# Kernel optimization log

Measured on AMD Instinct MI355X. Metric: run time of the kernel, lower is better.

Reference implementation:

```python
import jax, jax.numpy as jnp
import numpy as np

B, S, D, H, FFN = 4, 1024, 1024, 16, 4096
DH = D // H
EPS = 1e-5
NEG = -1e20


def _layer_norm(t, g, b):
    m = jnp.mean(t, axis=-1, keepdims=True)
    v = jnp.mean((t - m) ** 2, axis=-1, keepdims=True)
    return (t - m) / jnp.sqrt(v + EPS) * g + b


def setup_inputs() -> dict:
    key = jax.random.key(0)
    ks = jax.random.split(key, 16)
    std_attn = np.sqrt(2.0 / (D + D)).astype(np.float32)  # xavier normal
    lim1 = np.sqrt(6.0 / (D + FFN)).astype(np.float32)    # xavier uniform
    inp = {
        'tensor': jax.random.normal(ks[0], (B, S, D), jnp.float32),
        'mask': jnp.ones((B, S), jnp.int32),
        'wq': jax.random.normal(ks[1], (D, D), jnp.float32) * std_attn,
        'bq': jnp.zeros((D,), jnp.float32),
        'wk': jax.random.normal(ks[2], (D, D), jnp.float32) * std_attn,
        'bk': jnp.zeros((D,), jnp.float32),
        'wv': jax.random.normal(ks[3], (D, D), jnp.float32) * std_attn,
        'bv': jnp.zeros((D,), jnp.float32),
        'wo': jax.random.normal(ks[4], (D, D), jnp.float32) * std_attn,
        'bo': jnp.zeros((D,), jnp.float32),
        'ln1_g': jnp.ones((D,), jnp.float32),
        'ln1_b': jnp.zeros((D,), jnp.float32),
        'w1': jax.random.uniform(ks[5], (FFN, D), jnp.float32, -lim1, lim1),
        'b1': jnp.zeros((FFN,), jnp.float32),
        'w2': jax.random.uniform(ks[6], (D, FFN), jnp.float32, -lim1, lim1),
        'b2': jnp.zeros((D,), jnp.float32),
        'ln2_g': jnp.ones((D,), jnp.float32),
        'ln2_b': jnp.zeros((D,), jnp.float32),
    }
    return inp


def reference(tensor, mask, wq, bq, wk, bk, wv, bv, wo, bo,
              ln1_g, ln1_b, w1, b1, w2, b2, ln2_g, ln2_b):
    x = tensor
    scale = jnp.sqrt(jnp.float32(DH))
    # QKV projections -> [B, S, H, DH]
    q = (x @ wq.T + bq).reshape(B, S, H, DH)
    k = (x @ wk.T + bk).reshape(B, S, H, DH)
    v = (x @ wv.T + bv).reshape(B, S, H, DH)
    # scores [B, H, Sq, Sk]
    scores = jnp.einsum('bqhd,bkhd->bhqk', q / scale, k)
    blocked = (mask == 0)[:, None, None, :]  # True -> block
    scores = jnp.where(blocked, NEG, scores)
    attn = jax.nn.softmax(scores.astype(jnp.float32), axis=-1).astype(x.dtype)
    ctx = jnp.einsum('bhqk,bkhd->bqhd', attn, v).reshape(B, S, D)
    attn_out = ctx @ wo.T + bo
    # post-LN (variant='aiayn')
    t = _layer_norm(x + attn_out, ln1_g, ln1_b)
    ffn = jax.nn.relu(t @ w1.T + b1) @ w2.T + b2
    t = _layer_norm(t + ffn, ln2_g, ln2_b)
    t = t * mask[:, :, None].astype(t.dtype)
    return t
```

## Files before the change

### kernel.cpp

```cpp
#include <hip/hip_runtime.h>

typedef __bf16 bf16x8 __attribute__((ext_vector_type(8)));
typedef __bf16 bf16x4 __attribute__((ext_vector_type(4)));
typedef float f32x4 __attribute__((ext_vector_type(4)));
typedef float f32x16 __attribute__((ext_vector_type(16)));

#define BB 4
#define SS 1024
#define DD 1024
#define HH 16
#define DHH 64
#define FFN 4096

__device__ __forceinline__ void gload_lds16(const void* g, void* lds) {
  __builtin_amdgcn_global_load_lds(
      (const __attribute__((address_space(1))) unsigned int*)g,
      (__attribute__((address_space(3))) unsigned int*)lds, 16, 0, 0);
}

__global__ __launch_bounds__(256) void cvt_all_kernel(
    const float* __restrict__ x, const float* __restrict__ wq, const float* __restrict__ wk,
    const float* __restrict__ wv, const float* __restrict__ wo, const float* __restrict__ w1,
    const float* __restrict__ w2, __bf16* __restrict__ xb, __bf16* __restrict__ wqkvb,
    __bf16* __restrict__ wob, __bf16* __restrict__ w1b, __bf16* __restrict__ w2b)
{
  int i = blockIdx.x * 256 + threadIdx.x;
  const float* src; __bf16* dst; int off;
  if (i < 524288)       { src = x;  dst = xb;              off = i; }
  else if (i < 655360)  { src = wq; dst = wqkvb;           off = i - 524288; }
  else if (i < 786432)  { src = wk; dst = wqkvb + 1048576; off = i - 655360; }
  else if (i < 917504)  { src = wv; dst = wqkvb + 2097152; off = i - 786432; }
  else if (i < 1048576) { src = wo; dst = wob;             off = i - 917504; }
  else if (i < 1572864) { src = w1; dst = w1b;             off = i - 1048576; }
  else                  { src = w2; dst = w2b;             off = i - 1572864; }
  float4 a = *(const float4*)(src + off * 8);
  float4 b = *(const float4*)(src + off * 8 + 4);
  bf16x8 v;
  v[0] = (__bf16)a.x; v[1] = (__bf16)a.y; v[2] = (__bf16)a.z; v[3] = (__bf16)a.w;
  v[4] = (__bf16)b.x; v[5] = (__bf16)b.y; v[6] = (__bf16)b.z; v[7] = (__bf16)b.w;
  *(bf16x8*)(dst + off * 8) = v;
}

template<int MODE>
__global__ __launch_bounds__(256, 2) void gemm_bt(
    const __bf16* __restrict__ A, const __bf16* __restrict__ Bw,
    const float* __restrict__ bias, const float* __restrict__ bias1, const float* __restrict__ bias2,
    const float* __restrict__ res, void* __restrict__ outp, void* __restrict__ out1,
    int M, int N, int K, int kLen, float scale)
{
  __shared__ __bf16 As[2][128 * 32];
  __shared__ __bf16 Bs[2][128 * 32];
  const int tid = threadIdx.x;
  const int wid = tid >> 6;
  const int lane = tid & 63;
  const int lr = lane & 15;
  const int lg = lane >> 4;

  const int gx = gridDim.x;
  const int nwg = gx * gridDim.y;
  const int wg = blockIdx.y * gx + blockIdx.x;
  const int swz = (wg & 7) * (nwg >> 3) + (wg >> 3);
  const int bm = (swz / gx) * 128;
  const int bn = (swz % gx) * 128;

  const int wm = (wid >> 1) * 64;
  const int wn = (wid & 1) * 64;

  int kBeg = 0, nk = K >> 5;
  if constexpr (MODE == 5) { kBeg = blockIdx.z * kLen; nk = kLen >> 5; }

  const int off = tid * 16;
  const int srow = off >> 6;
  const int scol = (off & 63) >> 1;
  const __bf16* gA0 = A + (size_t)(bm + srow) * K + kBeg + scol;
  const __bf16* gA1 = A + (size_t)(bm + 64 + srow) * K + kBeg + scol;
  const __bf16* gB0 = Bw + (size_t)(bn + srow) * K + kBeg + scol;
  const __bf16* gB1 = Bw + (size_t)(bn + 64 + srow) * K + kBeg + scol;
  char* lA = (char*)&As[0][0] + wid * 1024;
  char* lB = (char*)&Bs[0][0] + wid * 1024;

  f32x4 acc[4][4] = {};

#define STAGE(buf, kk) do { \
    gload_lds16(gA0 + (kk), lA + (buf) * 8192); \
    gload_lds16(gA1 + (kk), lA + (buf) * 8192 + 4096); \
    gload_lds16(gB0 + (kk), lB + (buf) * 8192); \
    gload_lds16(gB1 + (kk), lB + (buf) * 8192 + 4096); \
  } while (0)

  STAGE(0, 0);
  __syncthreads();
  for (int t = 0; t < nk; ++t) {
    const int cur = t & 1;
    if (t + 1 < nk) STAGE(cur ^ 1, (t + 1) << 5);
    bf16x8 af[4], bv[4];
#pragma unroll
    for (int i = 0; i < 4; ++i)
      af[i] = *(const bf16x8*)&As[cur][(wm + i * 16 + lr) * 32 + lg * 8];
#pragma unroll
    for (int i = 0; i < 4; ++i)
      bv[i] = *(const bf16x8*)&Bs[cur][(wn + i * 16 + lr) * 32 + lg * 8];
#pragma unroll
    for (int i = 0; i < 4; ++i)
#pragma unroll
      for (int j = 0; j < 4; ++j)
        acc[i][j] = __builtin_amdgcn_mfma_f32_16x16x32_bf16(af[i], bv[j], acc[i][j], 0, 0, 0);
    __syncthreads();
  }
#undef STAGE

#pragma unroll
  for (int i = 0; i < 4; ++i) {
#pragma unroll
    for (int j = 0; j < 4; ++j) {
#pragma unroll
      for (int r = 0; r < 4; ++r) {
        int row = bm + wm + i * 16 + lg * 4 + r;
        int col = bn + wn + j * 16 + lr;
        float v = acc[i][j][r];
        if constexpr (MODE == 3) {
          float t2 = v + bias[col];
          ((__bf16*)outp)[(size_t)row * N + col] = (__bf16)fmaxf(t2, 0.f);
        } else if constexpr (MODE == 4) {
          int region = col >> 10;
          int col_ = col & 1023;
          int b_ = row >> 10, s_ = row & 1023;
          int h_ = col_ >> 6, d_ = col_ & 63;
          if (region == 0) {
            float v2 = (v + bias[col_]) * scale;
            ((__bf16*)outp)[(((size_t)(b_ * HH + h_) * SS) + s_) * DHH + d_] = (__bf16)v2;
          } else if (region == 1) {
            float v2 = v + bias1[col_];
            ((__bf16*)out1)[(((size_t)(b_ * HH + h_) * SS) + s_) * DHH + d_] = (__bf16)v2;
          } else {
            float v2 = v + bias2[col_];
            ((__bf16*)res)[(((size_t)(b_ * HH + h_) * DHH) + d_) * SS + s_] = (__bf16)v2;
          }
        } else if constexpr (MODE == 5) {
          float* dst = blockIdx.z ? (float*)out1 : (float*)outp;
          dst[(size_t)row * N + col] = v;
        } else if constexpr (MODE == 6) {
          size_t idx = (size_t)row * N + col;
          ((__bf16*)outp)[idx] = (__bf16)(v + bias[col] + res[idx]);
        }
      }
    }
  }
}

__global__ __launch_bounds__(256, 2) void attn_kernel(
    const __bf16* __restrict__ q, const __bf16* __restrict__ k,
    const __bf16* __restrict__ vt, const int* __restrict__ mask,
    __bf16* __restrict__ ctx)
{
  const int nwg = gridDim.x;
  const int wg = blockIdx.x;
  const int swzb = (wg & 7) * (nwg >> 3) + (wg >> 3);
  const int bh = swzb >> 3;
  const int qb = (swzb & 7) << 7;
  const int b = bh >> 4;

  const int tid = threadIdx.x, wid = tid >> 6, lane = tid & 63;
  const int ln = lane & 31, hi = lane >> 5;

  __shared__ __bf16 Kt[2][64 * 64];
  __shared__ __bf16 Vt[2][64 * 64];
  __shared__ __bf16 Pt[4][32 * 64];
  __shared__ float mmulLds[SS];

  {
    const int* mrow = mask + b * SS;
    int c = tid * 4;
    float4 mm;
    mm.x = (float)(mrow[c + 0] != 0);
    mm.y = (float)(mrow[c + 1] != 0);
    mm.z = (float)(mrow[c + 2] != 0);
    mm.w = (float)(mrow[c + 3] != 0);
    ((float4*)mmulLds)[tid] = mm;
  }

  const __bf16* qh = q + (size_t)bh * SS * DHH;
  const __bf16* kh = k + (size_t)bh * SS * DHH;
  const __bf16* vh = vt + (size_t)bh * DHH * SS;

  const int qw = qb + wid * 32;
  bf16x8 qf[4];
#pragma unroll
  for (int s = 0; s < 4; ++s)
    qf[s] = *(const bf16x8*)&qh[(size_t)(qw + ln) * DHH + s * 16 + hi * 8];

  const int srow = tid >> 3;
  const int ps = tid & 7;
  const int sw0 = (srow ^ (srow >> 3)) & 7;
  const int r1 = srow + 32;
  const int sw1 = (r1 ^ (r1 >> 3)) & 7;
  const __bf16* kS0 = kh + (size_t)srow * DHH + ((ps ^ sw0) * 8);
  const __bf16* kS1 = kh + (size_t)r1 * DHH + ((ps ^ sw1) * 8);
  const __bf16* vS0 = vh + (size_t)srow * SS + ((ps ^ sw0) * 8);
  const __bf16* vS1 = vh + (size_t)r1 * SS + ((ps ^ sw1) * 8);

#define ASTAGE(bufi, kb_) do { \
    gload_lds16(kS0 + (size_t)(kb_) * DHH, (char*)&Kt[bufi][0] + wid * 1024); \
    gload_lds16(kS1 + (size_t)(kb_) * DHH, (char*)&Kt[bufi][0] + wid * 1024 + 4096); \
    gload_lds16(vS0 + (kb_), (char*)&Vt[bufi][0] + wid * 1024); \
    gload_lds16(vS1 + (kb_), (char*)&Vt[bufi][0] + wid * 1024 + 4096); \
  } while (0)

  char* Pw = (char*)&Pt[wid][0];
  const int swA = (ln ^ (ln >> 3)) & 7;
  const int swB = swA ^ 4;

  f32x16 o0 = {}, o1 = {};
  float l[16];
#pragma unroll
  for (int r = 0; r < 16; ++r) l[r] = 0.f;

  ASTAGE(0, 0);
  __syncthreads();

#pragma unroll 1
  for (int t = 0; t < SS / 64; ++t) {
    const int cur = t & 1;
    const int kb = t * 64;
    if (t + 1 < SS / 64) ASTAGE(cur ^ 1, kb + 64);

    const char* Kc = (const char*)&Kt[cur][0];
    const char* Vc = (const char*)&Vt[cur][0];

    f32x16 sc0 = {}, sc1 = {};
#pragma unroll
    for (int s = 0; s < 4; ++s) {
      bf16x8 kb0 = *(const bf16x8*)(Kc + ln * 128 + (((s * 2 + hi) ^ swA) << 4));
      bf16x8 kb1 = *(const bf16x8*)(Kc + (32 + ln) * 128 + (((s * 2 + hi) ^ swB) << 4));
      sc0 = __builtin_amdgcn_mfma_f32_32x32x16_bf16(qf[s], kb0, sc0, 0, 0, 0);
      sc1 = __builtin_amdgcn_mfma_f32_32x32x16_bf16(qf[s], kb1, sc1, 0, 0, 0);
    }

    float mm0 = mmulLds[kb + ln];
    float mm1 = mmulLds[kb + 32 + ln];
#pragma unroll
    for (int r = 0; r < 16; ++r) {
      float p0 = exp2f(sc0[r] - 23.0831207f) * mm0;
      float p1 = exp2f(sc1[r] - 23.0831207f) * mm1;
      l[r] += p0 + p1;
      int qrow = (r & 3) + 8 * (r >> 2) + 4 * hi;
      int swq = (qrow ^ (qrow >> 3)) & 7;
      *(__bf16*)(Pw + qrow * 128 + ((((ln >> 3) + 0) ^ swq) << 4) + (ln & 7) * 2) = (__bf16)p0;
      *(__bf16*)(Pw + qrow * 128 + ((((ln >> 3) + 4) ^ swq) << 4) + (ln & 7) * 2) = (__bf16)p1;
    }

#pragma unroll
    for (int ks = 0; ks < 4; ++ks) {
      bf16x8 pa = *(const bf16x8*)(Pw + ln * 128 + (((ks * 2 + hi) ^ swA) << 4));
      bf16x8 vb0 = *(const bf16x8*)(Vc + ln * 128 + (((ks * 2 + hi) ^ swA) << 4));
      bf16x8 vb1 = *(const bf16x8*)(Vc + (32 + ln) * 128 + (((ks * 2 + hi) ^ swB) << 4));
      o0 = __builtin_amdgcn_mfma_f32_32x32x16_bf16(pa, vb0, o0, 0, 0, 0);
      o1 = __builtin_amdgcn_mfma_f32_32x32x16_bf16(pa, vb1, o1, 0, 0, 0);
    }
    __syncthreads();
  }
#undef ASTAGE

#pragma unroll
  for (int r = 0; r < 16; ++r) {
#pragma unroll
    for (int off = 1; off < 32; off <<= 1) l[r] += __shfl_xor(l[r], off);
  }

#pragma unroll
  for (int r = 0; r < 16; ++r) {
    float inv = l[r] > 0.f ? 1.f / l[r] : 0.f;
    int qrow = (r & 3) + 8 * (r >> 2) + 4 * hi;
    size_t base = ((size_t)b * SS + qw + qrow) * DD + (size_t)(bh & 15) * DHH;
    ctx[base + ln] = (__bf16)(o0[r] * inv);
    ctx[base + 32 + ln] = (__bf16)(o1[r] * inv);
  }
}

__global__ __launch_bounds__(256) void ln_bf16_kernel(
    const __bf16* __restrict__ in, const float* __restrict__ g, const float* __restrict__ b,
    __bf16* __restrict__ out16)
{
  int row = blockIdx.x;
  int tid = threadIdx.x;
  int wid = tid >> 6, lane = tid & 63;
  bf16x4 raw = ((const bf16x4*)(in + (size_t)row * DD))[tid];
  float4 v;
  v.x = (float)raw[0]; v.y = (float)raw[1]; v.z = (float)raw[2]; v.w = (float)raw[3];
  float s = v.x + v.y + v.z + v.w;
  float sq = v.x * v.x + v.y * v.y + v.z * v.z + v.w * v.w;
#pragma unroll
  for (int o = 1; o < 64; o <<= 1) { s += __shfl_xor(s, o); sq += __shfl_xor(sq, o); }
  __shared__ float red[8];
  if (lane == 0) { red[wid] = s; red[4 + wid] = sq; }
  __syncthreads();
  s = red[0] + red[1] + red[2] + red[3];
  sq = red[4] + red[5] + red[6] + red[7];
  float mean = s * (1.f / DD);
  float var = sq * (1.f / DD) - mean * mean;
  float rstd = rsqrtf(var + 1e-5f);
  float4 gg = ((const float4*)g)[tid];
  float4 bb = ((const float4*)b)[tid];
  bf16x4 w;
  w[0] = (__bf16)((v.x - mean) * rstd * gg.x + bb.x);
  w[1] = (__bf16)((v.y - mean) * rstd * gg.y + bb.y);
  w[2] = (__bf16)((v.z - mean) * rstd * gg.z + bb.z);
  w[3] = (__bf16)((v.w - mean) * rstd * gg.w + bb.w);
  *(bf16x4*)(out16 + (size_t)row * DD + tid * 4) = w;
}

__global__ __launch_bounds__(256) void ln2_fused_kernel(
    const float* __restrict__ p0, const float* __restrict__ p1, const float* __restrict__ bias,
    const __bf16* __restrict__ res, const float* __restrict__ g, const float* __restrict__ b,
    const int* __restrict__ mask, float* __restrict__ out)
{
  int row = blockIdx.x;
  int tid = threadIdx.x;
  int wid = tid >> 6, lane = tid & 63;
  size_t base = (size_t)row * DD;
  float4 a0 = ((const float4*)(p0 + base))[tid];
  float4 a1 = ((const float4*)(p1 + base))[tid];
  bf16x4 rw = ((const bf16x4*)(res + base))[tid];
  float4 bs = ((const float4*)bias)[tid];
  float4 v;
  v.x = a0.x + a1.x + (float)rw[0] + bs.x;
  v.y = a0.y + a1.y + (float)rw[1] + bs.y;
  v.z = a0.z + a1.z + (float)rw[2] + bs.z;
  v.w = a0.w + a1.w + (float)rw[3] + bs.w;
  float s = v.x + v.y + v.z + v.w;
  float sq = v.x * v.x + v.y * v.y + v.z * v.z + v.w * v.w;
#pragma unroll
  for (int o = 1; o < 64; o <<= 1) { s += __shfl_xor(s, o); sq += __shfl_xor(sq, o); }
  __shared__ float red[8];
  if (lane == 0) { red[wid] = s; red[4 + wid] = sq; }
  __syncthreads();
  s = red[0] + red[1] + red[2] + red[3];
  sq = red[4] + red[5] + red[6] + red[7];
  float mean = s * (1.f / DD);
  float var = sq * (1.f / DD) - mean * mean;
  float rstd = rsqrtf(var + 1e-5f);
  float4 gg = ((const float4*)g)[tid];
  float4 bb = ((const float4*)b)[tid];
  float mk = (float)mask[row];
  float4 o;
  o.x = ((v.x - mean) * rstd * gg.x + bb.x) * mk;
  o.y = ((v.y - mean) * rstd * gg.y + bb.y) * mk;
  o.z = ((v.z - mean) * rstd * gg.z + bb.z) * mk;
  o.w = ((v.w - mean) * rstd * gg.w + bb.w) * mk;
  ((float4*)(out + base))[tid] = o;
}

extern "C" void kernel_launch(void* const* d_in, const int* in_sizes, int n_in,
                              void* d_out, int out_size, void* d_ws, size_t ws_size,
                              hipStream_t stream) {
  const float* x    = (const float*)d_in[0];
  const int*  mask  = (const int*)d_in[1];
  const float* wq   = (const float*)d_in[2];
  const float* bq   = (const float*)d_in[3];
  const float* wk   = (const float*)d_in[4];
  const float* bk   = (const float*)d_in[5];
  const float* wv   = (const float*)d_in[6];
  const float* bv   = (const float*)d_in[7];
  const float* wo   = (const float*)d_in[8];
  const float* bo   = (const float*)d_in[9];
  const float* ln1g = (const float*)d_in[10];
  const float* ln1b = (const float*)d_in[11];
  const float* w1   = (const float*)d_in[12];
  const float* b1   = (const float*)d_in[13];
  const float* w2   = (const float*)d_in[14];
  const float* b2   = (const float*)d_in[15];
  const float* ln2g = (const float*)d_in[16];
  const float* ln2b = (const float*)d_in[17];
  float* out = (float*)d_out;
  char* ws = (char*)d_ws;

  __bf16* xb    = (__bf16*)(ws + 0);
  __bf16* wqkvb = (__bf16*)(ws + 8388608);
  __bf16* wob   = (__bf16*)(ws + 14680064);
  __bf16* w1b   = (__bf16*)(ws + 16777216);
  __bf16* w2b   = (__bf16*)(ws + 25165824);
  __bf16* qbuf  = (__bf16*)(ws + 33554432);
  __bf16* kbuf  = (__bf16*)(ws + 41943040);
  __bf16* vtbf  = (__bf16*)(ws + 50331648);
  __bf16* ctxb  = (__bf16*)(ws + 58720256);
  __bf16* hb    = (__bf16*)(ws + 33554432);
  __bf16* r1b   = (__bf16*)(ws + 67108864);
  float*  p0    = (float*)(ws + 83886080);
  __bf16* tb    = (__bf16*)(ws + 100663296);
  float*  p1    = (float*)(ws + 0);

  const int MSD = BB * SS;

  cvt_all_kernel<<<8192, 256, 0, stream>>>(x, wq, wk, wv, wo, w1, w2, xb, wqkvb, wob, w1b, w2b);

  gemm_bt<4><<<dim3(24, 32), 256, 0, stream>>>(xb, wqkvb, bq, bk, bv, (const float*)vtbf,
                                               qbuf, kbuf, MSD, 3072, DD, 0, 0.18033688f);

  attn_kernel<<<BB * HH * (SS / 128), 256, 0, stream>>>(qbuf, kbuf, vtbf, mask, ctxb);

  gemm_bt<6><<<dim3(8, 32), 256, 0, stream>>>(ctxb, wob, bo, nullptr, nullptr, x,
                                              r1b, nullptr, MSD, DD, DD, 0, 1.0f);
  ln_bf16_kernel<<<MSD, 256, 0, stream>>>(r1b, ln1g, ln1b, tb);

  gemm_bt<3><<<dim3(32, 32), 256, 0, stream>>>(tb, w1b, b1, nullptr, nullptr, nullptr,
                                               hb, nullptr, MSD, FFN, DD, 0, 1.0f);

  gemm_bt<5><<<dim3(8, 32, 2), 256, 0, stream>>>(hb, w2b, nullptr, nullptr, nullptr, nullptr,
                                                 p0, p1, MSD, DD, FFN, 2048, 1.0f);
  ln2_fused_kernel<<<MSD, 256, 0, stream>>>(p0, p1, b2, tb, ln2g, ln2b, mask, out);
}
```

Measured before the change: 231.9 us.

## Widen GEMM tiles to 128x256 with 512-thread blocks for QKV and FFN

Adds a gemm_wide kernel using 8 waves per block and a 128x256 output tile, with the B tile doubled in LDS. It is used for the QKV, FFN1 and FFN2 GEMMs to raise A-tile reuse and cut global traffic per FLOP. The output-projection GEMM keeps the old 128x128 tile as a separate gemm_wo kernel. The trade-off is fewer workgroups (for example 256 for FFN2), more LDS per block and possibly lower occupancy or uneven load across CUs.

Result: slower. 242.5 us (+4.6%).

```diff
diff --git a/kernel.cpp b/kernel.cpp
--- a/kernel.cpp
+++ b/kernel.cpp
@@ -42,14 +42,14 @@
 }
 
 template<int MODE>
-__global__ __launch_bounds__(256, 2) void gemm_bt(
+__global__ __launch_bounds__(512, 2) void gemm_wide(
     const __bf16* __restrict__ A, const __bf16* __restrict__ Bw,
     const float* __restrict__ bias, const float* __restrict__ bias1, const float* __restrict__ bias2,
     const float* __restrict__ res, void* __restrict__ outp, void* __restrict__ out1,
     int M, int N, int K, int kLen, float scale)
 {
   __shared__ __bf16 As[2][128 * 32];
-  __shared__ __bf16 Bs[2][128 * 32];
+  __shared__ __bf16 Bs[2][256 * 32];
   const int tid = threadIdx.x;
   const int wid = tid >> 6;
   const int lane = tid & 63;
@@ -61,31 +61,28 @@
   const int wg = blockIdx.y * gx + blockIdx.x;
   const int swz = (wg & 7) * (nwg >> 3) + (wg >> 3);
   const int bm = (swz / gx) * 128;
-  const int bn = (swz % gx) * 128;
-
-  const int wm = (wid >> 1) * 64;
-  const int wn = (wid & 1) * 64;
+  const int bn = (swz % gx) * 256;
+
+  const int wm = (wid >> 2) * 64;
+  const int wn = (wid & 3) * 64;
 
   int kBeg = 0, nk = K >> 5;
   if constexpr (MODE == 5) { kBeg = blockIdx.z * kLen; nk = kLen >> 5; }
 
-  const int off = tid * 16;
-  const int srow = off >> 6;
-  const int scol = (off & 63) >> 1;
-  const __bf16* gA0 = A + (size_t)(bm + srow) * K + kBeg + scol;
-  const __bf16* gA1 = A + (size_t)(bm + 64 + srow) * K + kBeg + scol;
-  const __bf16* gB0 = Bw + (size_t)(bn + srow) * K + kBeg + scol;
-  const __bf16* gB1 = Bw + (size_t)(bn + 64 + srow) * K + kBeg + scol;
+  const int sra = tid >> 2;
+  const int sca = (tid & 3) << 3;
+  const __bf16* gA  = A + (size_t)(bm + sra) * K + kBeg + sca;
+  const __bf16* gB0 = Bw + (size_t)(bn + sra) * K + kBeg + sca;
+  const __bf16* gB1 = Bw + (size_t)(bn + 128 + sra) * K + kBeg + sca;
   char* lA = (char*)&As[0][0] + wid * 1024;
   char* lB = (char*)&Bs[0][0] + wid * 1024;
 
   f32x4 acc[4][4] = {};
 
 #define STAGE(buf, kk) do { \
-    gload_lds16(gA0 + (kk), lA + (buf) * 8192); \
-    gload_lds16(gA1 + (kk), lA + (buf) * 8192 + 4096); \
-    gload_lds16(gB0 + (kk), lB + (buf) * 8192); \
-    gload_lds16(gB1 + (kk), lB + (buf) * 8192 + 4096); \
+    gload_lds16(gA + (kk), lA + (buf) * 8192); \
+    gload_lds16(gB0 + (kk), lB + (buf) * 16384); \
+    gload_lds16(gB1 + (kk), lB + (buf) * 16384 + 8192); \
   } while (0)
 
   STAGE(0, 0);
@@ -139,7 +136,88 @@
         } else if constexpr (MODE == 5) {
           float* dst = blockIdx.z ? (float*)out1 : (float*)outp;
           dst[(size_t)row * N + col] = v;
-        } else if constexpr (MODE == 6) {
+        }
+      }
+    }
+  }
+}
+
+template<int MODE>
+__global__ __launch_bounds__(256, 2) void gemm_wo(
+    const __bf16* __restrict__ A, const __bf16* __restrict__ Bw,
+    const float* __restrict__ bias, const float* __restrict__ res,
+    void* __restrict__ outp, int M, int N, int K)
+{
+  __shared__ __bf16 As[2][128 * 32];
+  __shared__ __bf16 Bs[2][128 * 32];
+  const int tid = threadIdx.x;
+  const int wid = tid >> 6;
+  const int lane = tid & 63;
+  const int lr = lane & 15;
+  const int lg = lane >> 4;
+
+  const int gx = gridDim.x;
+  const int nwg = gx * gridDim.y;
+  const int wg = blockIdx.y * gx + blockIdx.x;
+  const int swz = (wg & 7) * (nwg >> 3) + (wg >> 3);
+  const int bm = (swz / gx) * 128;
+  const int bn = (swz % gx) * 128;
+
+  const int wm = (wid >> 1) * 64;
+  const int wn = (wid & 1) * 64;
+
+  const int nk = K >> 5;
+
+  const int off = tid * 16;
+  const int srow = off >> 6;
+  const int scol = (off & 63) >> 1;
+  const __bf16* gA0 = A + (size_t)(bm + srow) * K + scol;
+  const __bf16* gA1 = A + (size_t)(bm + 64 + srow) * K + scol;
+  const __bf16* gB0 = Bw + (size_t)(bn + srow) * K + scol;
+  const __bf16* gB1 = Bw + (size_t)(bn + 64 + srow) * K + scol;
+  char* lA = (char*)&As[0][0] + wid * 1024;
+  char* lB = (char*)&Bs[0][0] + wid * 1024;
+
+  f32x4 acc[4][4] = {};
+
+#define STAGE(buf, kk) do { \
+    gload_lds16(gA0 + (kk), lA + (buf) * 8192); \
+    gload_lds16(gA1 + (kk), lA + (buf) * 8192 + 4096); \
+    gload_lds16(gB0 + (kk), lB + (buf) * 8192); \
+    gload_lds16(gB1 + (kk), lB + (buf) * 8192 + 4096); \
+  } while (0)
+
+  STAGE(0, 0);
+  __syncthreads();
+  for (int t = 0; t < nk; ++t) {
+    const int cur = t & 1;
+    if (t + 1 < nk) STAGE(cur ^ 1, (t + 1) << 5);
+    bf16x8 af[4], bv[4];
+#pragma unroll
+    for (int i = 0; i < 4; ++i)
+      af[i] = *(const bf16x8*)&As[cur][(wm + i * 16 + lr) * 32 + lg * 8];
+#pragma unroll
+    for (int i = 0; i < 4; ++i)
+      bv[i] = *(const bf16x8*)&Bs[cur][(wn + i * 16 + lr) * 32 + lg * 8];
+#pragma unroll
+    for (int i = 0; i < 4; ++i)
+#pragma unroll
+      for (int j = 0; j < 4; ++j)
+        acc[i][j] = __builtin_amdgcn_mfma_f32_16x16x32_bf16(af[i], bv[j], acc[i][j], 0, 0, 0);
+    __syncthreads();
+  }
+#undef STAGE
+
+#pragma unroll
+  for (int i = 0; i < 4; ++i) {
+#pragma unroll
+    for (int j = 0; j < 4; ++j) {
+#pragma unroll
+      for (int r = 0; r < 4; ++r) {
+        int row = bm + wm + i * 16 + lg * 4 + r;
+        int col = bn + wn + j * 16 + lr;
+        float v = acc[i][j][r];
+        if constexpr (MODE == 6) {
           size_t idx = (size_t)row * N + col;
           ((__bf16*)outp)[idx] = (__bf16)(v + bias[col] + res[idx]);
         }
@@ -393,19 +471,18 @@
 
   cvt_all_kernel<<<8192, 256, 0, stream>>>(x, wq, wk, wv, wo, w1, w2, xb, wqkvb, wob, w1b, w2b);
 
-  gemm_bt<4><<<dim3(24, 32), 256, 0, stream>>>(xb, wqkvb, bq, bk, bv, (const float*)vtbf,
-                                               qbuf, kbuf, MSD, 3072, DD, 0, 0.18033688f);
+  gemm_wide<4><<<dim3(12, 32), 512, 0, stream>>>(xb, wqkvb, bq, bk, bv, (const float*)vtbf,
+                                                 qbuf, kbuf, MSD, 3072, DD, 0, 0.18033688f);
 
   attn_kernel<<<BB * HH * (SS / 128), 256, 0, stream>>>(qbuf, kbuf, vtbf, mask, ctxb);
 
-  gemm_bt<6><<<dim3(8, 32), 256, 0, stream>>>(ctxb, wob, bo, nullptr, nullptr, x,
-                                              r1b, nullptr, MSD, DD, DD, 0, 1.0f);
+  gemm_wo<6><<<dim3(8, 32), 256, 0, stream>>>(ctxb, wob, bo, x, r1b, MSD, DD, DD);
   ln_bf16_kernel<<<MSD, 256, 0, stream>>>(r1b, ln1g, ln1b, tb);
 
-  gemm_bt<3><<<dim3(32, 32), 256, 0, stream>>>(tb, w1b, b1, nullptr, nullptr, nullptr,
-                                               hb, nullptr, MSD, FFN, DD, 0, 1.0f);
-
-  gemm_bt<5><<<dim3(8, 32, 2), 256, 0, stream>>>(hb, w2b, nullptr, nullptr, nullptr, nullptr,
-                                                 p0, p1, MSD, DD, FFN, 2048, 1.0f);
+  gemm_wide<3><<<dim3(16, 32), 512, 0, stream>>>(tb, w1b, b1, nullptr, nullptr, nullptr,
+                                                 hb, nullptr, MSD, FFN, DD, 0, 1.0f);
+
+  gemm_wide<5><<<dim3(4, 32, 2), 512, 0, stream>>>(hb, w2b, nullptr, nullptr, nullptr, nullptr,
+                                                   p0, p1, MSD, DD, FFN, 2048, 1.0f);
   ln2_fused_kernel<<<MSD, 256, 0, stream>>>(p0, p1, b2, tb, ln2g, ln2b, mask, out);
 }
```
